# Optimization experiments

Hardware: AMD Instinct MI355X
Metric: run time of the kernel (lower is better)

## Reference

```python
import jax, jax.numpy as jnp
import numpy as np

IMSIZE = 128; R = 2; B = 2; C = 3; D = 64; Q = 128; M = 8; ITERS = 32
N = IMSIZE * IMSIZE
EPS = 1e-8


def _build_edges(S, r):
    # local (2r+1)^2 pixel neighborhood, as in build_perception(imsize, perception_size)
    ys, xs = np.meshgrid(np.arange(S), np.arange(S), indexing='ij')
    rows, cols = [], []
    for dy in range(-r, r + 1):
        for dx in range(-r, r + 1):
            ny, nx = ys + dy, xs + dx
            ok = (ny >= 0) & (ny < S) & (nx >= 0) & (nx < S)
            rows.append((ys * S + xs)[ok])
            cols.append((ny * S + nx)[ok])
    return (np.concatenate(rows).astype(np.int32), np.concatenate(cols).astype(np.int32))


def _conv(x, w, b=None):
    y = jax.lax.conv_general_dilated(x, w, (1, 1), 'SAME', dimension_numbers=('NHWC', 'HWIO', 'NHWC'))
    return y if b is None else y + b


def _bn(x, g, b):
    mu = x.mean((0, 1, 2))
    var = x.var((0, 1, 2))
    return (x - mu) * jax.lax.rsqrt(var + 1e-5) * g + b


def _resblock(f, w1, g1, t1, w2, g2, t2):
    h = jax.nn.relu(_bn(_conv(f, w1), g1, t1))
    h = _bn(_conv(h, w2), g2, t2)
    return jax.nn.relu(f + h)


def _forward(x, w_bb1, b_bb1, w_bb2, b_bb2,
             w_k1, g_k1, t_k1, w_k2, g_k2, t_k2, w_kp, b_kp,
             w_q1, g_q1, t_q1, w_q2, g_q2, t_q2, w_qp,
             h0, row, col, agent_idx):
    # conv backbone (preserves spatial resolution)
    f = jax.nn.relu(_conv(x, w_bb1, b_bb1))
    f = jax.nn.relu(_conv(f, w_bb2, b_bb2))
    # key / query heads: ResidualBlock + 1x1 conv
    ks = _conv(_resblock(f, w_k1, g_k1, t_k1, w_k2, g_k2, t_k2), w_kp, b_kp).reshape(B, N, D)
    qs = _conv(_resblock(f, w_q1, g_q1, t_q1, w_q2, g_q2, t_q2), w_qp).reshape(B, N, D)
    # edge-gather cosine similarity (torch.cosine_similarity with eps=1e-8)
    qe = qs[:, row]          # [B, E, D]
    ke = ks[:, col]          # [B, E, D]
    weights = (qe * ke).sum(-1) / (
        jnp.maximum(jnp.linalg.norm(qe, axis=-1), EPS) *
        jnp.maximum(jnp.linalg.norm(ke, axis=-1), EPS))   # [B, E]

    # 32-iteration sparse adjacency propagation: h <- normalize(A @ h)
    def step(h, _):
        msg = jnp.zeros_like(h).at[:, row, :].add(weights[:, :, None] * h[:, col, :])
        h = msg / jnp.maximum(jnp.linalg.norm(msg, axis=-1, keepdims=True), EPS)
        return h, None

    h, _ = jax.lax.scan(step, h0, None, length=ITERS)     # [B, N, Q]

    # competition routing: pixels compete for M agent slots via cosine affinity
    pix = h / jnp.maximum(jnp.linalg.norm(h, axis=-1, keepdims=True), EPS)
    ag = pix[:, agent_idx]                                # [B, M, Q]
    sim = jnp.einsum('bnq,bmq->bnm', pix, ag)
    masks = jax.nn.softmax(sim * 10.0, axis=-1)           # [B, N, M]
    return masks.reshape(B, IMSIZE, IMSIZE, M).transpose(0, 3, 1, 2)  # [B, M, W, H]


def setup_inputs() -> dict:
    key = jax.random.key(0)
    k = jax.random.split(key, 12)
    s = 0.05
    row, col = _build_edges(IMSIZE, R)
    agent_idx = np.linspace(0, N - 1, M).astype(np.int32)
    return dict(
        x=jax.random.normal(k[0], (B, IMSIZE, IMSIZE, C), jnp.float32),
        w_bb1=jax.random.normal(k[1], (3, 3, C, D), jnp.float32) * s, b_bb1=jnp.zeros((D,), jnp.float32),
        w_bb2=jax.random.normal(k[2], (3, 3, D, D), jnp.float32) * s, b_bb2=jnp.zeros((D,), jnp.float32),
        w_k1=jax.random.normal(k[3], (3, 3, D, D), jnp.float32) * s,
        g_k1=jnp.ones((D,), jnp.float32), t_k1=jnp.zeros((D,), jnp.float32),
        w_k2=jax.random.normal(k[4], (3, 3, D, D), jnp.float32) * s,
        g_k2=jnp.ones((D,), jnp.float32), t_k2=jnp.zeros((D,), jnp.float32),
        w_kp=jax.random.normal(k[5], (1, 1, D, D), jnp.float32) * s, b_kp=jnp.zeros((D,), jnp.float32),
        w_q1=jax.random.normal(k[6], (3, 3, D, D), jnp.float32) * s,
        g_q1=jnp.ones((D,), jnp.float32), t_q1=jnp.zeros((D,), jnp.float32),
        w_q2=jax.random.normal(k[7], (3, 3, D, D), jnp.float32) * s,
        g_q2=jnp.ones((D,), jnp.float32), t_q2=jnp.zeros((D,), jnp.float32),
        w_qp=jax.random.normal(k[8], (1, 1, D, D), jnp.float32) * s,
        h0=jax.random.normal(k[9], (B, N, Q), jnp.float32),
        row=jnp.asarray(row), col=jnp.asarray(col),
        agent_idx=jnp.asarray(agent_idx),
    )


def reference(x, w_bb1, b_bb1, w_bb2, b_bb2,
              w_k1, g_k1, t_k1, w_k2, g_k2, t_k2, w_kp, b_kp,
              w_q1, g_q1, t_q1, w_q2, g_q2, t_q2, w_qp,
              h0, row, col, agent_idx):
    return _forward(x, w_bb1, b_bb1, w_bb2, b_bb2,
                    w_k1, g_k1, t_k1, w_k2, g_k2, t_k2, w_kp, b_kp,
                    w_q1, g_q1, t_q1, w_q2, g_q2, t_q2, w_qp,
                    h0, row, col, agent_idx)
```

## Files before the change

### kernel.cpp

```cpp
#include <hip/hip_runtime.h>
#include <math.h>

#define NPIX 16384
#define EPSF 1e-8f

typedef float f32x4 __attribute__((ext_vector_type(4)));
typedef short s16x8 __attribute__((ext_vector_type(8)));

__device__ __forceinline__ float wred64(float s){
  s += __shfl_xor(s, 32); s += __shfl_xor(s, 16); s += __shfl_xor(s, 8);
  s += __shfl_xor(s, 4);  s += __shfl_xor(s, 2);  s += __shfl_xor(s, 1);
  return s;
}
__device__ __forceinline__ float rdlane(float v, int l){
  return __int_as_float(__builtin_amdgcn_readlane(__float_as_int(v), l));
}
__device__ __forceinline__ float dot4f(float4 a, float4 b, float acc){
  acc = fmaf(a.x,b.x,acc); acc = fmaf(a.y,b.y,acc);
  acc = fmaf(a.z,b.z,acc); acc = fmaf(a.w,b.w,acc);
  return acc;
}
__device__ __forceinline__ void bf16split(float v, unsigned short &hi, unsigned short &lo){
  unsigned u = __float_as_uint(v);
  unsigned r = u + 0x7FFFu + ((u >> 16) & 1u);
  hi = (unsigned short)(r >> 16);
  float hf = __uint_as_float(((unsigned)hi) << 16);
  float l = v - hf;
  unsigned u2 = __float_as_uint(l);
  unsigned r2 = u2 + 0x7FFFu + ((u2 >> 16) & 1u);
  lo = (unsigned short)(r2 >> 16);
}

__global__ __launch_bounds__(256) void prep_kernel(const float* __restrict__ w_bb2, const float* __restrict__ w_k1,
                            const float* __restrict__ w_k2, const float* __restrict__ w_q1,
                            const float* __restrict__ w_q2, const float* __restrict__ w_kp,
                            const float* __restrict__ w_qp, unsigned short* __restrict__ wh,
                            unsigned short* __restrict__ wl, float* __restrict__ wtp,
                            float* __restrict__ stats){
  int gid = blockIdx.x*256 + threadIdx.x;
  if (gid < 184320){
    int j = gid & 7;
    int t1 = gid >> 3;
    int lane = t1 & 63;
    int t2 = t1 >> 6;
    int kb = t2 % 18;
    int t3 = t2 / 18;
    int ct = t3 & 3;
    int c  = t3 >> 2;
    const float* src = c==0? w_bb2 : c==1? w_k1 : c==2? w_k2 : c==3? w_q1 : w_q2;
    int cout = ct*16 + (lane & 15);
    int k = kb*32 + (lane>>4)*8 + j;
    float v = src[k*64 + cout];
    unsigned short h,l; bf16split(v,h,l);
    wh[gid] = h; wl[gid] = l;
  } else if (gid < 192512){
    int t = gid - 184320; int which = t >> 12; int d = t & 4095;
    const float* src = which ? w_qp : w_kp;
    int k = d & 3, cout = (d>>2) & 63, cin4 = d >> 8;
    wtp[t] = src[(cin4*4 + k)*64 + cout];
  } else if (gid < 193024){
    stats[gid - 192512] = 0.f;
  }
}

__global__ __launch_bounds__(256) void conv1_kernel(const float* __restrict__ x, const float* __restrict__ w,
                                                    const float* __restrict__ bias, float* __restrict__ out){
  int wv = blockIdx.x*4 + (threadIdx.x >> 6);
  int c  = threadIdx.x & 63;
  int p0 = wv << 3;
  int ub = __builtin_amdgcn_readfirstlane(p0);
  int b  = ub >> 14; int i0 = ub & (NPIX-1);
  int y  = i0 >> 7, x0 = i0 & 127;
  float wv_[9][3];
  #pragma unroll
  for (int t=0;t<9;++t)
    #pragma unroll
    for (int ci=0;ci<3;++ci) wv_[t][ci] = w[(t*3+ci)*64 + c];
  float bv = bias[c];
  float acc[8];
  #pragma unroll
  for (int p=0;p<8;++p) acc[p] = bv;
  for (int ky=0; ky<3; ++ky){
    int ny = y + ky - 1;
    if ((unsigned)ny >= 128u) continue;
    const float* rowp = x + ((b<<14) + ny*128)*3;
    for (int kx=0; kx<3; ++kx){
      int t = ky*3 + kx;
      #pragma unroll
      for (int p=0;p<8;++p){
        int col = x0 + p + kx - 1;
        if ((unsigned)col < 128u){
          const float* ip = rowp + col*3;
          acc[p] = fmaf(ip[0], wv_[t][0], acc[p]);
          acc[p] = fmaf(ip[1], wv_[t][1], acc[p]);
          acc[p] = fmaf(ip[2], wv_[t][2], acc[p]);
        }
      }
    }
  }
  float* op = out + (p0 << 6) + c;
  #pragma unroll
  for (int p=0;p<8;++p) op[p*64] = fmaxf(acc[p], 0.f);
}

__global__ __launch_bounds__(512) void conv3m_kernel(const float* __restrict__ in,
    const unsigned short* __restrict__ wh, const unsigned short* __restrict__ wl,
    const float* __restrict__ bias, int relu,
    const float* __restrict__ bnst, const float* __restrict__ bng, const float* __restrict__ bnb,
    float* __restrict__ out, float* __restrict__ ost){
  __shared__ unsigned short lhi[12672];
  __shared__ unsigned short llo[12672];
  __shared__ float lout[4352];
  __shared__ float la[64], lb[64];
  __shared__ float ls1[64], ls2[64];
  int blk = blockIdx.x;
  int xh = blk & 1, y = (blk>>1) & 127, b = blk >> 8;
  int x0 = xh << 6;
  int tid = threadIdx.x;
  if (tid < 64){
    float a = 1.f, bo = 0.f;
    if (bnst){
      float mu  = bnst[tid] * (1.f/32768.f);
      float var = bnst[64+tid] * (1.f/32768.f) - mu*mu;
      a  = bng[tid] * rsqrtf(var + 1e-5f);
      bo = bnb[tid] - mu*a;
    }
    la[tid] = a; lb[tid] = bo;
    ls1[tid] = 0.f; ls2[tid] = 0.f;
  }
  __syncthreads();
  for (int s = tid; s < 3168; s += 512){
    int pr = s >> 4, cq = s & 15;
    int ky = pr / 66, px = pr - ky*66;
    int ny = y + ky - 1, gx = x0 - 1 + px;
    float v0=0.f, v1=0.f, v2=0.f, v3=0.f;
    if ((unsigned)ny < 128u && (unsigned)gx < 128u){
      const float* ip = in + (((b<<14) + ny*128 + gx)<<6) + (cq<<2);
      float4 t = *(const float4*)ip;
      int c0 = cq<<2;
      v0 = fmaxf(fmaf(t.x, la[c0],   lb[c0]),   0.f);
      v1 = fmaxf(fmaf(t.y, la[c0+1], lb[c0+1]), 0.f);
      v2 = fmaxf(fmaf(t.z, la[c0+2], lb[c0+2]), 0.f);
      v3 = fmaxf(fmaf(t.w, la[c0+3], lb[c0+3]), 0.f);
    }
    unsigned short h0,l0,h1,l1,h2,l2,h3,l3;
    bf16split(v0,h0,l0); bf16split(v1,h1,l1); bf16split(v2,h2,l2); bf16split(v3,h3,l3);
    int slot = (cq >> 1) ^ (pr & 7);
    int byte = pr*128 + (slot<<4) + ((cq & 1) << 3);
    *(uint2*)((char*)lhi + byte) = make_uint2((unsigned)h0 | ((unsigned)h1<<16),
                                              (unsigned)h2 | ((unsigned)h3<<16));
    *(uint2*)((char*)llo + byte) = make_uint2((unsigned)l0 | ((unsigned)l1<<16),
                                              (unsigned)l2 | ((unsigned)l3<<16));
  }
  __syncthreads();
  int lane = tid & 63, wid = tid >> 6;
  int pxsub = wid & 3, ch = wid >> 2;
  int col16 = lane & 15, kgrp = lane >> 4;
  f32x4 acc0 = {0.f,0.f,0.f,0.f}, acc1 = acc0, acl0 = acc0, acl1 = acc0;
  int abase = (ch*2*18)*512 + lane*8;
  #pragma unroll
  for (int kb=0; kb<18; ++kb){
    int tap = kb >> 1;
    int ky = (tap >= 6) ? 2 : (tap >= 3 ? 1 : 0);
    int kx = tap - ky*3;
    int pr = ky*66 + pxsub*16 + col16 + kx;
    int ci0 = ((kb & 1) << 5) + (kgrp << 3);
    int byte = pr*128 + ((((ci0 >> 3) ^ (pr & 7))) << 4);
    s16x8 Bh = *(const s16x8*)((const char*)lhi + byte);
    s16x8 Bl = *(const s16x8*)((const char*)llo + byte);
    int ao = abase + kb*512;
    s16x8 Ah0 = *(const s16x8*)(wh + ao);
    s16x8 Al0 = *(const s16x8*)(wl + ao);
    s16x8 Ah1 = *(const s16x8*)(wh + ao + 9216);
    s16x8 Al1 = *(const s16x8*)(wl + ao + 9216);
    acc0 = __builtin_amdgcn_mfma_f32_16x16x32_bf16(Ah0, Bh, acc0, 0, 0, 0);
    acl0 = __builtin_amdgcn_mfma_f32_16x16x32_bf16(Ah0, Bl, acl0, 0, 0, 0);
    acc1 = __builtin_amdgcn_mfma_f32_16x16x32_bf16(Ah1, Bh, acc1, 0, 0, 0);
    acl1 = __builtin_amdgcn_mfma_f32_16x16x32_bf16(Ah1, Bl, acl1, 0, 0, 0);
    acl0 = __builtin_amdgcn_mfma_f32_16x16x32_bf16(Al0, Bh, acl0, 0, 0, 0);
    acl1 = __builtin_amdgcn_mfma_f32_16x16x32_bf16(Al1, Bh, acl1, 0, 0, 0);
  }
  acc0 = acc0 + acl0;
  acc1 = acc1 + acl1;
  int pxl = pxsub*16 + col16;
  int co0 = ch*32 + kgrp*4;
  *(f32x4*)(lout + pxl*68 + co0)      = acc0;
  *(f32x4*)(lout + pxl*68 + co0 + 16) = acc1;
  __syncthreads();
  {
    int px = tid >> 3, c8 = (tid & 7) << 3;
    const float* lp = lout + px*68 + c8;
    float r0[8];
    #pragma unroll
    for (int j=0;j<8;++j) r0[j] = lp[j];
    if (bias){
      #pragma unroll
      for (int j=0;j<8;++j) r0[j] += bias[c8+j];
    }
    if (relu){
      #pragma unroll
      for (int j=0;j<8;++j) r0[j] = fmaxf(r0[j], 0.f);
    }
    float* op = out + (((b<<14) + y*128 + x0 + px)<<6) + c8;
    #pragma unroll
    for (int j=0;j<8;++j) op[j] = r0[j];
    if (ost){
      float s1v[8], s2v[8];
      #pragma unroll
      for (int j=0;j<8;++j){ s1v[j] = r0[j]; s2v[j] = r0[j]*r0[j]; }
      #pragma unroll
      for (int m=8; m<64; m<<=1){
        #pragma unroll
        for (int j=0;j<8;++j){ s1v[j] += __shfl_xor(s1v[j], m); s2v[j] += __shfl_xor(s2v[j], m); }
      }
      int lane2 = tid & 63;
      if ((lane2 >> 3) == 0){
        int c0 = (lane2 & 7) << 3;
        #pragma unroll
        for (int j=0;j<8;++j){ atomicAdd(&ls1[c0+j], s1v[j]); atomicAdd(&ls2[c0+j], s2v[j]); }
      }
      __syncthreads();
      if (tid < 64){ atomicAdd(&ost[tid], ls1[tid]); atomicAdd(&ost[64+tid], ls2[tid]); }
    }
  }
}

__global__ __launch_bounds__(512) void conv3m2_kernel(const float* __restrict__ in,
    const unsigned short* __restrict__ whA, const unsigned short* __restrict__ wlA,
    const unsigned short* __restrict__ whB, const unsigned short* __restrict__ wlB,
    float* __restrict__ outA, float* __restrict__ ostA,
    float* __restrict__ outB, float* __restrict__ ostB){
  __shared__ unsigned short lhi[12672];
  __shared__ unsigned short llo[12672];
  __shared__ float lout[4352];
  __shared__ float ls1A[64], ls2A[64], ls1B[64], ls2B[64];
  int blk = blockIdx.x;
  int xh = blk & 1, y = (blk>>1) & 127, b = blk >> 8;
  int x0 = xh << 6;
  int tid = threadIdx.x;
  if (tid < 64){ ls1A[tid]=0.f; ls2A[tid]=0.f; ls1B[tid]=0.f; ls2B[tid]=0.f; }
  __syncthreads();
  for (int s = tid; s < 3168; s += 512){
    int pr = s >> 4, cq = s & 15;
    int ky = pr / 66, px = pr - ky*66;
    int ny = y + ky - 1, gx = x0 - 1 + px;
    float v0=0.f, v1=0.f, v2=0.f, v3=0.f;
    if ((unsigned)ny < 128u && (unsigned)gx < 128u){
      const float* ip = in + (((b<<14) + ny*128 + gx)<<6) + (cq<<2);
      float4 t = *(const float4*)ip;
      v0 = t.x; v1 = t.y; v2 = t.z; v3 = t.w;
    }
    unsigned short h0,l0,h1,l1,h2,l2,h3,l3;
    bf16split(v0,h0,l0); bf16split(v1,h1,l1); bf16split(v2,h2,l2); bf16split(v3,h3,l3);
    int slot = (cq >> 1) ^ (pr & 7);
    int byte = pr*128 + (slot<<4) + ((cq & 1) << 3);
    *(uint2*)((char*)lhi + byte) = make_uint2((unsigned)h0 | ((unsigned)h1<<16),
                                              (unsigned)h2 | ((unsigned)h3<<16));
    *(uint2*)((char*)llo + byte) = make_uint2((unsigned)l0 | ((unsigned)l1<<16),
                                              (unsigned)l2 | ((unsigned)l3<<16));
  }
  __syncthreads();
  int lane = tid & 63, wid = tid >> 6;
  int pxsub = wid & 3, ch = wid >> 2;
  int col16 = lane & 15, kgrp = lane >> 4;
  f32x4 z = {0.f,0.f,0.f,0.f};
  f32x4 aA0=z, aA1=z, lA0=z, lA1=z, aB0=z, aB1=z, lB0=z, lB1=z;
  int abase = (ch*2*18)*512 + lane*8;
  #pragma unroll
  for (int kb=0; kb<18; ++kb){
    int tap = kb >> 1;
    int ky = (tap >= 6) ? 2 : (tap >= 3 ? 1 : 0);
    int kx = tap - ky*3;
    int pr = ky*66 + pxsub*16 + col16 + kx;
    int ci0 = ((kb & 1) << 5) + (kgrp << 3);
    int byte = pr*128 + ((((ci0 >> 3) ^ (pr & 7))) << 4);
    s16x8 Bh = *(const s16x8*)((const char*)lhi + byte);
    s16x8 Bl = *(const s16x8*)((const char*)llo + byte);
    int ao = abase + kb*512;
    s16x8 AhA0 = *(const s16x8*)(whA + ao);
    s16x8 AlA0 = *(const s16x8*)(wlA + ao);
    s16x8 AhA1 = *(const s16x8*)(whA + ao + 9216);
    s16x8 AlA1 = *(const s16x8*)(wlA + ao + 9216);
    s16x8 AhB0 = *(const s16x8*)(whB + ao);
    s16x8 AlB0 = *(const s16x8*)(wlB + ao);
    s16x8 AhB1 = *(const s16x8*)(whB + ao + 9216);
    s16x8 AlB1 = *(const s16x8*)(wlB + ao + 9216);
    aA0 = __builtin_amdgcn_mfma_f32_16x16x32_bf16(AhA0, Bh, aA0, 0, 0, 0);
    lA0 = __builtin_amdgcn_mfma_f32_16x16x32_bf16(AhA0, Bl, lA0, 0, 0, 0);
    aA1 = __builtin_amdgcn_mfma_f32_16x16x32_bf16(AhA1, Bh, aA1, 0, 0, 0);
    lA1 = __builtin_amdgcn_mfma_f32_16x16x32_bf16(AhA1, Bl, lA1, 0, 0, 0);
    lA0 = __builtin_amdgcn_mfma_f32_16x16x32_bf16(AlA0, Bh, lA0, 0, 0, 0);
    lA1 = __builtin_amdgcn_mfma_f32_16x16x32_bf16(AlA1, Bh, lA1, 0, 0, 0);
    aB0 = __builtin_amdgcn_mfma_f32_16x16x32_bf16(AhB0, Bh, aB0, 0, 0, 0);
    lB0 = __builtin_amdgcn_mfma_f32_16x16x32_bf16(AhB0, Bl, lB0, 0, 0, 0);
    aB1 = __builtin_amdgcn_mfma_f32_16x16x32_bf16(AhB1, Bh, aB1, 0, 0, 0);
    lB1 = __builtin_amdgcn_mfma_f32_16x16x32_bf16(AhB1, Bl, lB1, 0, 0, 0);
    lB0 = __builtin_amdgcn_mfma_f32_16x16x32_bf16(AlB0, Bh, lB0, 0, 0, 0);
    lB1 = __builtin_amdgcn_mfma_f32_16x16x32_bf16(AlB1, Bh, lB1, 0, 0, 0);
  }
  aA0 = aA0 + lA0; aA1 = aA1 + lA1;
  aB0 = aB0 + lB0; aB1 = aB1 + lB1;
  int pxl = pxsub*16 + col16;
  int co0 = ch*32 + kgrp*4;
  int px = tid >> 3, c8 = (tid & 7) << 3;
  int lane2 = tid & 63;
  #pragma unroll
  for (int phase=0; phase<2; ++phase){
    f32x4 w0 = phase ? aB0 : aA0;
    f32x4 w1 = phase ? aB1 : aA1;
    float* outp = phase ? outB : outA;
    float* ostp = phase ? ostB : ostA;
    float* lsp1 = phase ? ls1B : ls1A;
    float* lsp2 = phase ? ls2B : ls2A;
    *(f32x4*)(lout + pxl*68 + co0)      = w0;
    *(f32x4*)(lout + pxl*68 + co0 + 16) = w1;
    __syncthreads();
    const float* lp = lout + px*68 + c8;
    float r0[8];
    #pragma unroll
    for (int j=0;j<8;++j) r0[j] = lp[j];
    float* op = outp + (((b<<14) + y*128 + x0 + px)<<6) + c8;
    #pragma unroll
    for (int j=0;j<8;++j) op[j] = r0[j];
    float s1v[8], s2v[8];
    #pragma unroll
    for (int j=0;j<8;++j){ s1v[j] = r0[j]; s2v[j] = r0[j]*r0[j]; }
    #pragma unroll
    for (int m=8; m<64; m<<=1){
      #pragma unroll
      for (int j=0;j<8;++j){ s1v[j] += __shfl_xor(s1v[j], m); s2v[j] += __shfl_xor(s2v[j], m); }
    }
    if ((lane2 >> 3) == 0){
      int c0 = (lane2 & 7) << 3;
      #pragma unroll
      for (int j=0;j<8;++j){ atomicAdd(&lsp1[c0+j], s1v[j]); atomicAdd(&lsp2[c0+j], s2v[j]); }
    }
    __syncthreads();
  }
  if (tid < 64){
    atomicAdd(&ostA[tid], ls1A[tid]); atomicAdd(&ostA[64+tid], ls2A[tid]);
    atomicAdd(&ostB[tid], ls1B[tid]); atomicAdd(&ostB[64+tid], ls2B[tid]);
  }
}

__global__ __launch_bounds__(256) void resfuse_kernel(float* __restrict__ t, const float* __restrict__ f,
                                                      const float* __restrict__ stats, const float* __restrict__ g,
                                                      const float* __restrict__ beta){
  int idx4 = blockIdx.x*256 + threadIdx.x;
  float4 v = ((float4*)t)[idx4];
  float4 fv = ((const float4*)f)[idx4];
  int c0 = (idx4 & 15) * 4;
  float a[4], bb[4];
  #pragma unroll
  for (int j=0;j<4;++j){
    int c = c0 + j;
    float mu  = stats[c]    * (1.f/32768.f);
    float var = stats[64+c] * (1.f/32768.f) - mu*mu;
    a[j]  = g[c] * rsqrtf(var + 1e-5f);
    bb[j] = beta[c] - mu*a[j];
  }
  v.x = fmaxf(fv.x + fmaf(v.x, a[0], bb[0]), 0.f);
  v.y = fmaxf(fv.y + fmaf(v.y, a[1], bb[1]), 0.f);
  v.z = fmaxf(fv.z + fmaf(v.z, a[2], bb[2]), 0.f);
  v.w = fmaxf(fv.w + fmaf(v.w, a[3], bb[3]), 0.f);
  ((float4*)t)[idx4] = v;
}

__global__ __launch_bounds__(256) void proj_kernel(const float* __restrict__ r, const float* __restrict__ wt1,
                                                   const float* __restrict__ bias, float* __restrict__ out,
                                                   float* __restrict__ nrm){
  int wv = blockIdx.x*4 + (threadIdx.x >> 6);
  int c  = threadIdx.x & 63;
  int p0 = wv << 3;
  int ub = __builtin_amdgcn_readfirstlane(p0);
  const float4* wq = (const float4*)wt1 + c;
  float4 w[16];
  #pragma unroll
  for (int q=0;q<16;++q) w[q] = wq[q*64];
  float bv = bias ? bias[c] : 0.f;
  #pragma unroll
  for (int p=0;p<8;++p){
    const float* ip = r + ((ub + p) << 6);
    float a0 = bv, a1 = 0.f;
    #pragma unroll
    for (int q=0;q<16;q+=2){
      float4 i0 = *(const float4*)(ip + (q<<2));
      float4 i1 = *(const float4*)(ip + ((q+1)<<2));
      a0 = dot4f(i0, w[q],   a0);
      a1 = dot4f(i1, w[q+1], a1);
    }
    float acc = a0 + a1;
    out[((p0+p)<<6) + c] = acc;
    float s = wred64(acc*acc);
    if (c == 0) nrm[p0+p] = sqrtf(s);
  }
}

#define EW_PAD 68
__global__ __launch_bounds__(256) void edge_kernel(const float* __restrict__ qs, const float* __restrict__ ks,
                                                   const float* __restrict__ nq, const float* __restrict__ nk,
                                                   float* __restrict__ W){
  __shared__ float klds[100*EW_PAD];
  __shared__ float qlds[16*EW_PAD];
  int blk = blockIdx.x;
  int b = blk >> 10; int rem = blk & 1023;
  int y = rem >> 3; int x0 = (rem & 7) << 4;
  int tid = threadIdx.x;
  for (int s = tid; s < 1600; s += 256){
    int cin4 = s & 15; int col = (s >> 4) % 20; int r = (s >> 4) / 20;
    int ry = y - 2 + r; ry = ry < 0 ? 0 : (ry > 127 ? 127 : ry);
    int cx = x0 - 2 + col; cx = cx < 0 ? 0 : (cx > 127 ? 127 : cx);
    float4 v = *(const float4*)(ks + (((b<<14) + ry*128 + cx)<<6) + cin4*4);
    *(float4*)(klds + (r*20+col)*EW_PAD + cin4*4) = v;
  }
  {
    int cin4 = tid & 15; int px = tid >> 4;
    float4 v = *(const float4*)(qs + (((b<<14) + y*128 + x0 + px)<<6) + cin4*4);
    *(float4*)(qlds + px*EW_PAD + cin4*4) = v;
  }
  __syncthreads();
  #pragma unroll
  for (int pair=0; pair<2; ++pair){
    int t2 = tid + pair*256;
    int px = t2 >> 5; int o = t2 & 31;
    if (o < 25){
      int dy = o/5 - 2, dx = o%5 - 2;
      int yy = y + dy, xx = x0 + px + dx;
      bool valid = ((unsigned)yy < 128u) && ((unsigned)xx < 128u);
      const float* kq = klds + ((dy+2)*20 + (px+dx+2))*EW_PAD;
      const float* qq = qlds + px*EW_PAD;
      float a0 = 0.f, a1 = 0.f;
      #pragma unroll
      for (int q=0; q<16; q+=2){
        a0 = dot4f(*(const float4*)(qq + q*4),     *(const float4*)(kq + q*4),     a0);
        a1 = dot4f(*(const float4*)(qq + (q+1)*4), *(const float4*)(kq + (q+1)*4), a1);
      }
      float acc = a0 + a1;
      int gp = (b<<14) + y*128 + x0 + px;
      float wv_ = 0.f;
      if (valid){
        int gj = (b<<14) + yy*128 + xx;
        float rq = 1.f / fmaxf(nq[gp], EPSF);
        float rk = 1.f / fmaxf(nk[gj], EPSF);
        wv_ = acc * rq * rk;
      }
      W[gp*25 + o] = wv_;
    }
  }
}

__global__ __launch_bounds__(256) void mp_iter_kernel(const float* __restrict__ src, float* __restrict__ dst,
                                                      const float* __restrict__ W){
  int lane = threadIdx.x & 63;
  int wid  = threadIdx.x >> 6;
  int blk  = blockIdx.x;
  int xcd = blk & 7, s = blk >> 3;
  int row_id = xcd*32 + (s >> 3);
  int q8 = s & 7;
  int b = row_id >> 7, y = row_id & 127;
  int x0 = ((q8 << 2) + wid) << 2;
  int gp0 = (b << 14) + y*128 + x0;
  int lo = lane < 25 ? lane : 24;
  float wv[4];
  #pragma unroll
  for (int p=0;p<4;++p) wv[p] = W[(gp0+p)*25 + lo];
  const float* rp[5];
  #pragma unroll
  for (int r=0;r<5;++r){
    int ry = y - 2 + r; ry = ry < 0 ? 0 : (ry > 127 ? 127 : ry);
    rp[r] = src + (((b<<14) + ry*128) << 7) + lane;
  }
  float wa[5][5], wb[5][5];
  #pragma unroll
  for (int cc=0; cc<4; ++cc){
    int xc = x0 - 2 + cc; if (xc < 0) xc = 0;
    int off = xc << 7;
    #pragma unroll
    for (int r=0;r<5;++r){ wa[r][cc] = rp[r][off]; wb[r][cc] = rp[r][off + 64]; }
  }
  #pragma unroll
  for (int p=0;p<4;++p){
    int xl = x0 + p + 2; if (xl > 127) xl = 127;
    int off = xl << 7;
    #pragma unroll
    for (int r=0;r<5;++r){ wa[r][4] = rp[r][off]; wb[r][4] = rp[r][off + 64]; }
    float a0 = 0.f, a1 = 0.f;
    #pragma unroll
    for (int r=0;r<5;++r){
      #pragma unroll
      for (int cc=0;cc<5;++cc){
        float w = rdlane(wv[p], r*5+cc);
        a0 = fmaf(w, wa[r][cc], a0);
        a1 = fmaf(w, wb[r][cc], a1);
      }
    }
    float ss = wred64(a0*a0 + a1*a1);
    float sc = 1.f / fmaxf(sqrtf(ss), EPSF);
    float* dp = dst + ((gp0 + p) << 7) + lane;
    dp[0] = a0*sc; dp[64] = a1*sc;
    #pragma unroll
    for (int r=0;r<5;++r){
      #pragma unroll
      for (int cc=0;cc<4;++cc){ wa[r][cc] = wa[r][cc+1]; wb[r][cc] = wb[r][cc+1]; }
    }
  }
}

__global__ __launch_bounds__(256) void mp_final_kernel(const float* __restrict__ hf, const int* __restrict__ agidx,
                                                       float* __restrict__ out){
  int lane = threadIdx.x & 63;
  int wid  = threadIdx.x >> 6;
  int blk  = blockIdx.x;
  int xcd = blk & 7, s = blk >> 3;
  int row_id = xcd*32 + (s >> 2);
  int q4 = s & 3;
  int b = row_id >> 7, y = row_id & 127;
  int x0 = ((q4 << 2) + wid) << 3;
  int gp0 = (b << 14) + y*128 + x0;
  float av0[8], av1[8], isc[8];
  #pragma unroll
  for (int m=0;m<8;++m){
    int ai = agidx[m];
    const float* ap = hf + (((b<<14) + ai) << 7) + lane;
    av0[m] = ap[0]; av1[m] = ap[64];
    float ssm = wred64(av0[m]*av0[m] + av1[m]*av1[m]);
    isc[m] = 1.f / fmaxf(sqrtf(ssm), EPSF);
  }
  #pragma unroll 1
  for (int p=0;p<8;++p){
    int gp = gp0 + p;
    const float* hp = hf + (gp << 7) + lane;
    float v0 = hp[0], v1 = hp[64];
    float ss = wred64(v0*v0 + v1*v1);
    float sc = 1.f / fmaxf(sqrtf(ss), EPSF);
    float p0 = v0*sc, p1 = v1*sc;
    float sim[8];
    #pragma unroll
    for (int m=0;m<8;++m)
      sim[m] = wred64(p0*av0[m] + p1*av1[m]) * isc[m];
    float mx = sim[0];
    #pragma unroll
    for (int m=1;m<8;++m) mx = fmaxf(mx, sim[m]);
    float e[8]; float sum = 0.f;
    #pragma unroll
    for (int m=0;m<8;++m){ e[m] = __expf((sim[m]-mx)*10.f); sum += e[m]; }
    float rs = 1.f / sum;
    if (lane < 8){
      float val = e[0];
      #pragma unroll
      for (int m=1;m<8;++m) val = (lane==m) ? e[m] : val;
      out[(((b<<3)+lane)<<14) + y*128 + x0 + p] = val * rs;
    }
  }
}

extern "C" void kernel_launch(void* const* d_in, const int* in_sizes, int n_in,
                              void* d_out, int out_size, void* d_ws, size_t ws_size,
                              hipStream_t stream) {
  (void)in_sizes; (void)n_in; (void)out_size; (void)ws_size;
  const float* x     = (const float*)d_in[0];
  const float* w_bb1 = (const float*)d_in[1];
  const float* b_bb1 = (const float*)d_in[2];
  const float* w_bb2 = (const float*)d_in[3];
  const float* b_bb2 = (const float*)d_in[4];
  const float* w_k1  = (const float*)d_in[5];
  const float* g_k1  = (const float*)d_in[6];
  const float* t_k1  = (const float*)d_in[7];
  const float* w_k2  = (const float*)d_in[8];
  const float* g_k2  = (const float*)d_in[9];
  const float* t_k2  = (const float*)d_in[10];
  const float* w_kp  = (const float*)d_in[11];
  const float* b_kp  = (const float*)d_in[12];
  const float* w_q1  = (const float*)d_in[13];
  const float* g_q1  = (const float*)d_in[14];
  const float* t_q1  = (const float*)d_in[15];
  const float* w_q2  = (const float*)d_in[16];
  const float* g_q2  = (const float*)d_in[17];
  const float* t_q2  = (const float*)d_in[18];
  const float* w_qp  = (const float*)d_in[19];
  const float* h0    = (const float*)d_in[20];
  const int*   agidx = (const int*)d_in[23];
  float* out = (float*)d_out;
  float* ws  = (float*)d_ws;

  float* S0 = ws + 0;
  float* S1 = ws + 2097152;
  float* S2 = ws + 4194304;
  float* S3 = ws + 6291456;
  float* S4 = ws + 8388608;
  float* WW = ws + 12582912;
  float* NK = ws + 13402112;
  float* NQ = ws + 13434880;
  float* ST = ws + 13467648;
  float* WTp = ws + 13470208;
  unsigned short* WH = (unsigned short*)(ws + 13478400);
  unsigned short* WL = WH + 184320;
  float* HA = ws + 0;
  float* HB = ws + 4194304;

  prep_kernel<<<754, 256, 0, stream>>>(w_bb2, w_k1, w_k2, w_q1, w_q2, w_kp, w_qp, WH, WL, WTp, ST);
  conv1_kernel<<<1024, 256, 0, stream>>>(x, w_bb1, b_bb1, S0);
  conv3m_kernel<<<512, 512, 0, stream>>>(S0, WH + 0, WL + 0, b_bb2, 1, nullptr, nullptr, nullptr, S1, nullptr);
  conv3m2_kernel<<<512, 512, 0, stream>>>(S1, WH + 36864, WL + 36864, WH + 3*36864, WL + 3*36864,
                                          S2, ST + 0, S3, ST + 256);
  conv3m_kernel<<<512, 512, 0, stream>>>(S2, WH + 2*36864, WL + 2*36864, nullptr, 0, ST + 0, g_k1, t_k1, S0, ST + 128);
  resfuse_kernel<<<2048, 256, 0, stream>>>(S0, S1, ST + 128, g_k2, t_k2);
  proj_kernel<<<1024, 256, 0, stream>>>(S0, WTp + 0, b_kp, S4, NK);
  conv3m_kernel<<<512, 512, 0, stream>>>(S3, WH + 4*36864, WL + 4*36864, nullptr, 0, ST + 256, g_q1, t_q1, S2, ST + 384);
  resfuse_kernel<<<2048, 256, 0, stream>>>(S2, S1, ST + 384, g_q2, t_q2);
  proj_kernel<<<1024, 256, 0, stream>>>(S2, WTp + 4096, nullptr, S3, NQ);
  edge_kernel<<<2048, 256, 0, stream>>>(S3, S4, NQ, NK, WW);
  const float* sbuf = h0;
  for (int it = 0; it < 32; ++it){
    float* dbuf = (it & 1) ? HB : HA;
    mp_iter_kernel<<<2048, 256, 0, stream>>>(sbuf, dbuf, WW);
    sbuf = dbuf;
  }
  mp_final_kernel<<<1024, 256, 0, stream>>>(HB, agidx, out);
}
```

Baseline: 605.5 us.

## Fuse last propagation step into final softmax and merge key/query epilogue kernels

Shrinks shared memory in the conv kernels by aliasing the bf16 staging buffers with the output tile, which adds an extra barrier. The key and query resfuse and projection kernels are merged into single launches. The 32nd message-passing iteration is folded into the final agent-similarity kernel, which recomputes the aggregated features for its pixels and agents directly from the previous state. This aims to cut launches and occupancy limits and to avoid one full write and read of the hidden state, at the cost of redundant neighbourhood gathers for the agent rows.

```diff
diff --git a/kernel.cpp b/kernel.cpp
--- a/kernel.cpp
+++ b/kernel.cpp
@@ -108,9 +108,9 @@
     const float* __restrict__ bias, int relu,
     const float* __restrict__ bnst, const float* __restrict__ bng, const float* __restrict__ bnb,
     float* __restrict__ out, float* __restrict__ ost){
-  __shared__ unsigned short lhi[12672];
-  __shared__ unsigned short llo[12672];
-  __shared__ float lout[4352];
+  __shared__ char smem[50688];
+  unsigned short* lhi = (unsigned short*)smem;
+  float* lout = (float*)smem;
   __shared__ float la[64], lb[64];
   __shared__ float ls1[64], ls2[64];
   int blk = blockIdx.x;
@@ -147,10 +147,10 @@
     bf16split(v0,h0,l0); bf16split(v1,h1,l1); bf16split(v2,h2,l2); bf16split(v3,h3,l3);
     int slot = (cq >> 1) ^ (pr & 7);
     int byte = pr*128 + (slot<<4) + ((cq & 1) << 3);
-    *(uint2*)((char*)lhi + byte) = make_uint2((unsigned)h0 | ((unsigned)h1<<16),
-                                              (unsigned)h2 | ((unsigned)h3<<16));
-    *(uint2*)((char*)llo + byte) = make_uint2((unsigned)l0 | ((unsigned)l1<<16),
-                                              (unsigned)l2 | ((unsigned)l3<<16));
+    *(uint2*)(smem + byte) = make_uint2((unsigned)h0 | ((unsigned)h1<<16),
+                                        (unsigned)h2 | ((unsigned)h3<<16));
+    *(uint2*)(smem + 25344 + byte) = make_uint2((unsigned)l0 | ((unsigned)l1<<16),
+                                                (unsigned)l2 | ((unsigned)l3<<16));
   }
   __syncthreads();
   int lane = tid & 63, wid = tid >> 6;
@@ -166,8 +166,8 @@
     int pr = ky*66 + pxsub*16 + col16 + kx;
     int ci0 = ((kb & 1) << 5) + (kgrp << 3);
     int byte = pr*128 + ((((ci0 >> 3) ^ (pr & 7))) << 4);
-    s16x8 Bh = *(const s16x8*)((const char*)lhi + byte);
-    s16x8 Bl = *(const s16x8*)((const char*)llo + byte);
+    s16x8 Bh = *(const s16x8*)(smem + byte);
+    s16x8 Bl = *(const s16x8*)(smem + 25344 + byte);
     int ao = abase + kb*512;
     s16x8 Ah0 = *(const s16x8*)(wh + ao);
     s16x8 Al0 = *(const s16x8*)(wl + ao);
@@ -182,6 +182,7 @@
   }
   acc0 = acc0 + acl0;
   acc1 = acc1 + acl1;
+  __syncthreads();
   int pxl = pxsub*16 + col16;
   int co0 = ch*32 + kgrp*4;
   *(f32x4*)(lout + pxl*68 + co0)      = acc0;
@@ -230,9 +231,9 @@
     const unsigned short* __restrict__ whB, const unsigned short* __restrict__ wlB,
     float* __restrict__ outA, float* __restrict__ ostA,
     float* __restrict__ outB, float* __restrict__ ostB){
-  __shared__ unsigned short lhi[12672];
-  __shared__ unsigned short llo[12672];
-  __shared__ float lout[4352];
+  __shared__ char smem[50688];
+  float* loutA = (float*)smem;
+  float* loutB = (float*)smem + 4352;
   __shared__ float ls1A[64], ls2A[64], ls1B[64], ls2B[64];
   int blk = blockIdx.x;
   int xh = blk & 1, y = (blk>>1) & 127, b = blk >> 8;
@@ -254,10 +255,10 @@
     bf16split(v0,h0,l0); bf16split(v1,h1,l1); bf16split(v2,h2,l2); bf16split(v3,h3,l3);
     int slot = (cq >> 1) ^ (pr & 7);
     int byte = pr*128 + (slot<<4) + ((cq & 1) << 3);
-    *(uint2*)((char*)lhi + byte) = make_uint2((unsigned)h0 | ((unsigned)h1<<16),
-                                              (unsigned)h2 | ((unsigned)h3<<16));
-    *(uint2*)((char*)llo + byte) = make_uint2((unsigned)l0 | ((unsigned)l1<<16),
-                                              (unsigned)l2 | ((unsigned)l3<<16));
+    *(uint2*)(smem + byte) = make_uint2((unsigned)h0 | ((unsigned)h1<<16),
+                                        (unsigned)h2 | ((unsigned)h3<<16));
+    *(uint2*)(smem + 25344 + byte) = make_uint2((unsigned)l0 | ((unsigned)l1<<16),
+                                                (unsigned)l2 | ((unsigned)l3<<16));
   }
   __syncthreads();
   int lane = tid & 63, wid = tid >> 6;
@@ -274,8 +275,8 @@
     int pr = ky*66 + pxsub*16 + col16 + kx;
     int ci0 = ((kb & 1) << 5) + (kgrp << 3);
     int byte = pr*128 + ((((ci0 >> 3) ^ (pr & 7))) << 4);
-    s16x8 Bh = *(const s16x8*)((const char*)lhi + byte);
-    s16x8 Bl = *(const s16x8*)((const char*)llo + byte);
+    s16x8 Bh = *(const s16x8*)(smem + byte);
+    s16x8 Bl = *(const s16x8*)(smem + 25344 + byte);
     int ao = abase + kb*512;
     s16x8 AhA0 = *(const s16x8*)(whA + ao);
     s16x8 AlA0 = *(const s16x8*)(wlA + ao);
@@ -300,53 +301,62 @@
   }
   aA0 = aA0 + lA0; aA1 = aA1 + lA1;
   aB0 = aB0 + lB0; aB1 = aB1 + lB1;
+  __syncthreads();
   int pxl = pxsub*16 + col16;
   int co0 = ch*32 + kgrp*4;
-  int px = tid >> 3, c8 = (tid & 7) << 3;
-  int lane2 = tid & 63;
-  #pragma unroll
-  for (int phase=0; phase<2; ++phase){
-    f32x4 w0 = phase ? aB0 : aA0;
-    f32x4 w1 = phase ? aB1 : aA1;
-    float* outp = phase ? outB : outA;
-    float* ostp = phase ? ostB : ostA;
-    float* lsp1 = phase ? ls1B : ls1A;
-    float* lsp2 = phase ? ls2B : ls2A;
-    *(f32x4*)(lout + pxl*68 + co0)      = w0;
-    *(f32x4*)(lout + pxl*68 + co0 + 16) = w1;
-    __syncthreads();
-    const float* lp = lout + px*68 + c8;
-    float r0[8];
-    #pragma unroll
-    for (int j=0;j<8;++j) r0[j] = lp[j];
-    float* op = outp + (((b<<14) + y*128 + x0 + px)<<6) + c8;
-    #pragma unroll
-    for (int j=0;j<8;++j) op[j] = r0[j];
-    float s1v[8], s2v[8];
-    #pragma unroll
-    for (int j=0;j<8;++j){ s1v[j] = r0[j]; s2v[j] = r0[j]*r0[j]; }
+  *(f32x4*)(loutA + pxl*68 + co0)      = aA0;
+  *(f32x4*)(loutA + pxl*68 + co0 + 16) = aA1;
+  *(f32x4*)(loutB + pxl*68 + co0)      = aB0;
+  *(f32x4*)(loutB + pxl*68 + co0 + 16) = aB1;
+  __syncthreads();
+  {
+    int px = tid >> 3, c8 = (tid & 7) << 3;
+    int lane2 = tid & 63;
+    float rA[8], rB[8];
+    #pragma unroll
+    for (int j=0;j<8;++j){ rA[j] = loutA[px*68 + c8 + j]; rB[j] = loutB[px*68 + c8 + j]; }
+    float* opA = outA + (((b<<14) + y*128 + x0 + px)<<6) + c8;
+    float* opB = outB + (((b<<14) + y*128 + x0 + px)<<6) + c8;
+    #pragma unroll
+    for (int j=0;j<8;++j){ opA[j] = rA[j]; opB[j] = rB[j]; }
+    float sA1[8], sA2[8], sB1[8], sB2[8];
+    #pragma unroll
+    for (int j=0;j<8;++j){ sA1[j]=rA[j]; sA2[j]=rA[j]*rA[j]; sB1[j]=rB[j]; sB2[j]=rB[j]*rB[j]; }
     #pragma unroll
     for (int m=8; m<64; m<<=1){
       #pragma unroll
-      for (int j=0;j<8;++j){ s1v[j] += __shfl_xor(s1v[j], m); s2v[j] += __shfl_xor(s2v[j], m); }
+      for (int j=0;j<8;++j){
+        sA1[j] += __shfl_xor(sA1[j], m); sA2[j] += __shfl_xor(sA2[j], m);
+        sB1[j] += __shfl_xor(sB1[j], m); sB2[j] += __shfl_xor(sB2[j], m);
+      }
     }
     if ((lane2 >> 3) == 0){
       int c0 = (lane2 & 7) << 3;
       #pragma unroll
-      for (int j=0;j<8;++j){ atomicAdd(&lsp1[c0+j], s1v[j]); atomicAdd(&lsp2[c0+j], s2v[j]); }
+      for (int j=0;j<8;++j){
+        atomicAdd(&ls1A[c0+j], sA1[j]); atomicAdd(&ls2A[c0+j], sA2[j]);
+        atomicAdd(&ls1B[c0+j], sB1[j]); atomicAdd(&ls2B[c0+j], sB2[j]);
+      }
     }
     __syncthreads();
-  }
-  if (tid < 64){
-    atomicAdd(&ostA[tid], ls1A[tid]); atomicAdd(&ostA[64+tid], ls2A[tid]);
-    atomicAdd(&ostB[tid], ls1B[tid]); atomicAdd(&ostB[64+tid], ls2B[tid]);
-  }
-}
-
-__global__ __launch_bounds__(256) void resfuse_kernel(float* __restrict__ t, const float* __restrict__ f,
-                                                      const float* __restrict__ stats, const float* __restrict__ g,
-                                                      const float* __restrict__ beta){
-  int idx4 = blockIdx.x*256 + threadIdx.x;
+    if (tid < 64){
+      atomicAdd(&ostA[tid], ls1A[tid]); atomicAdd(&ostA[64+tid], ls2A[tid]);
+      atomicAdd(&ostB[tid], ls1B[tid]); atomicAdd(&ostB[64+tid], ls2B[tid]);
+    }
+  }
+}
+
+__global__ __launch_bounds__(256) void resfuse2_kernel(float* __restrict__ tk, float* __restrict__ tq,
+                                                       const float* __restrict__ f, const float* __restrict__ ST,
+                                                       const float* __restrict__ gk, const float* __restrict__ bk,
+                                                       const float* __restrict__ gq, const float* __restrict__ bq){
+  int gid = blockIdx.x*256 + threadIdx.x;
+  int isQ = gid >> 19;
+  int idx4 = gid & 524287;
+  float* t = isQ ? tq : tk;
+  const float* stats = ST + (isQ ? 384 : 128);
+  const float* g    = isQ ? gq : gk;
+  const float* beta = isQ ? bq : bk;
   float4 v = ((float4*)t)[idx4];
   float4 fv = ((const float4*)f)[idx4];
   int c0 = (idx4 & 15) * 4;
@@ -366,18 +376,25 @@
   ((float4*)t)[idx4] = v;
 }
 
-__global__ __launch_bounds__(256) void proj_kernel(const float* __restrict__ r, const float* __restrict__ wt1,
-                                                   const float* __restrict__ bias, float* __restrict__ out,
-                                                   float* __restrict__ nrm){
-  int wv = blockIdx.x*4 + (threadIdx.x >> 6);
+__global__ __launch_bounds__(256) void proj2_kernel(const float* __restrict__ rk, const float* __restrict__ rq,
+                                                    const float* __restrict__ wtp, const float* __restrict__ bkp,
+                                                    float* __restrict__ outk, float* __restrict__ outq,
+                                                    float* __restrict__ nk, float* __restrict__ nq){
+  int wvg = blockIdx.x*4 + (threadIdx.x >> 6);
+  int isQ = wvg >> 12;
+  int wv = wvg & 4095;
   int c  = threadIdx.x & 63;
+  const float* r = isQ ? rq : rk;
+  const float* wt1 = wtp + (isQ ? 4096 : 0);
+  float* out = isQ ? outq : outk;
+  float* nrm = isQ ? nq : nk;
   int p0 = wv << 3;
   int ub = __builtin_amdgcn_readfirstlane(p0);
   const float4* wq = (const float4*)wt1 + c;
   float4 w[16];
   #pragma unroll
   for (int q=0;q<16;++q) w[q] = wq[q*64];
-  float bv = bias ? bias[c] : 0.f;
+  float bv = isQ ? 0.f : bkp[c];
   #pragma unroll
   for (int p=0;p<8;++p){
     const float* ip = r + ((ub + p) << 6);
@@ -506,8 +523,8 @@
   }
 }
 
-__global__ __launch_bounds__(256) void mp_final_kernel(const float* __restrict__ hf, const int* __restrict__ agidx,
-                                                       float* __restrict__ out){
+__global__ __launch_bounds__(256) void mp_last_kernel(const float* __restrict__ src, const float* __restrict__ W,
+                                                      const int* __restrict__ agidx, float* __restrict__ out){
   int lane = threadIdx.x & 63;
   int wid  = threadIdx.x >> 6;
   int blk  = blockIdx.x;
@@ -517,23 +534,66 @@
   int b = row_id >> 7, y = row_id & 127;
   int x0 = ((q4 << 2) + wid) << 3;
   int gp0 = (b << 14) + y*128 + x0;
+  int lo = lane < 25 ? lane : 24;
   float av0[8], av1[8], isc[8];
   #pragma unroll
   for (int m=0;m<8;++m){
     int ai = agidx[m];
-    const float* ap = hf + (((b<<14) + ai) << 7) + lane;
-    av0[m] = ap[0]; av1[m] = ap[64];
-    float ssm = wred64(av0[m]*av0[m] + av1[m]*av1[m]);
+    int ay = ai >> 7, ax = ai & 127;
+    float wva = W[((b<<14) + ai)*25 + lo];
+    float aa0 = 0.f, aa1 = 0.f;
+    #pragma unroll
+    for (int r=0;r<5;++r){
+      int ry = ay - 2 + r; ry = ry < 0 ? 0 : (ry > 127 ? 127 : ry);
+      const float* rp = src + (((b<<14) + ry*128) << 7) + lane;
+      #pragma unroll
+      for (int cc=0;cc<5;++cc){
+        int xc = ax - 2 + cc; xc = xc < 0 ? 0 : (xc > 127 ? 127 : xc);
+        float w = rdlane(wva, r*5+cc);
+        aa0 = fmaf(w, rp[xc<<7], aa0);
+        aa1 = fmaf(w, rp[(xc<<7) + 64], aa1);
+      }
+    }
+    float ssm = wred64(aa0*aa0 + aa1*aa1);
     isc[m] = 1.f / fmaxf(sqrtf(ssm), EPSF);
-  }
-  #pragma unroll 1
+    av0[m] = aa0; av1[m] = aa1;
+  }
+  float wv[8];
+  #pragma unroll
+  for (int p=0;p<8;++p) wv[p] = W[(gp0+p)*25 + lo];
+  const float* rp[5];
+  #pragma unroll
+  for (int r=0;r<5;++r){
+    int ry = y - 2 + r; ry = ry < 0 ? 0 : (ry > 127 ? 127 : ry);
+    rp[r] = src + (((b<<14) + ry*128) << 7) + lane;
+  }
+  float wa[5][5], wb[5][5];
+  #pragma unroll
+  for (int cc=0; cc<4; ++cc){
+    int xc = x0 - 2 + cc; if (xc < 0) xc = 0;
+    int off = xc << 7;
+    #pragma unroll
+    for (int r=0;r<5;++r){ wa[r][cc] = rp[r][off]; wb[r][cc] = rp[r][off + 64]; }
+  }
+  #pragma unroll
   for (int p=0;p<8;++p){
-    int gp = gp0 + p;
-    const float* hp = hf + (gp << 7) + lane;
-    float v0 = hp[0], v1 = hp[64];
-    float ss = wred64(v0*v0 + v1*v1);
+    int xl = x0 + p + 2; if (xl > 127) xl = 127;
+    int off = xl << 7;
+    #pragma unroll
+    for (int r=0;r<5;++r){ wa[r][4] = rp[r][off]; wb[r][4] = rp[r][off + 64]; }
+    float a0 = 0.f, a1 = 0.f;
+    #pragma unroll
+    for (int r=0;r<5;++r){
+      #pragma unroll
+      for (int cc=0;cc<5;++cc){
+        float w = rdlane(wv[p], r*5+cc);
+        a0 = fmaf(w, wa[r][cc], a0);
+        a1 = fmaf(w, wb[r][cc], a1);
+      }
+    }
+    float ss = wred64(a0*a0 + a1*a1);
     float sc = 1.f / fmaxf(sqrtf(ss), EPSF);
-    float p0 = v0*sc, p1 = v1*sc;
+    float p0 = a0*sc, p1 = a1*sc;
     float sim[8];
     #pragma unroll
     for (int m=0;m<8;++m)
@@ -550,6 +610,11 @@
       #pragma unroll
       for (int m=1;m<8;++m) val = (lane==m) ? e[m] : val;
       out[(((b<<3)+lane)<<14) + y*128 + x0 + p] = val * rs;
+    }
+    #pragma unroll
+    for (int r=0;r<5;++r){
+      #pragma unroll
+      for (int cc=0;cc<4;++cc){ wa[r][cc] = wa[r][cc+1]; wb[r][cc] = wb[r][cc+1]; }
     }
   }
 }
@@ -604,17 +669,15 @@
   conv3m2_kernel<<<512, 512, 0, stream>>>(S1, WH + 36864, WL + 36864, WH + 3*36864, WL + 3*36864,
                                           S2, ST + 0, S3, ST + 256);
   conv3m_kernel<<<512, 512, 0, stream>>>(S2, WH + 2*36864, WL + 2*36864, nullptr, 0, ST + 0, g_k1, t_k1, S0, ST + 128);
-  resfuse_kernel<<<2048, 256, 0, stream>>>(S0, S1, ST + 128, g_k2, t_k2);
-  proj_kernel<<<1024, 256, 0, stream>>>(S0, WTp + 0, b_kp, S4, NK);
   conv3m_kernel<<<512, 512, 0, stream>>>(S3, WH + 4*36864, WL + 4*36864, nullptr, 0, ST + 256, g_q1, t_q1, S2, ST + 384);
-  resfuse_kernel<<<2048, 256, 0, stream>>>(S2, S1, ST + 384, g_q2, t_q2);
-  proj_kernel<<<1024, 256, 0, stream>>>(S2, WTp + 4096, nullptr, S3, NQ);
+  resfuse2_kernel<<<4096, 256, 0, stream>>>(S0, S2, S1, ST, g_k2, t_k2, g_q2, t_q2);
+  proj2_kernel<<<2048, 256, 0, stream>>>(S0, S2, WTp, b_kp, S4, S3, NK, NQ);
   edge_kernel<<<2048, 256, 0, stream>>>(S3, S4, NQ, NK, WW);
   const float* sbuf = h0;
-  for (int it = 0; it < 32; ++it){
+  for (int it = 0; it < 31; ++it){
     float* dbuf = (it & 1) ? HB : HA;
     mp_iter_kernel<<<2048, 256, 0, stream>>>(sbuf, dbuf, WW);
     sbuf = dbuf;
   }
-  mp_final_kernel<<<1024, 256, 0, stream>>>(HB, agidx, out);
-}
+  mp_last_kernel<<<1024, 256, 0, stream>>>(HA, WW, agidx, out);
+}
```

Result: no change. 612.2 us (+1.1%).
